# Kernel tuning notes

Hardware: AMD Instinct MI355X
Metric: run time of the kernel (lower is better)

Reference implementation:

```python
import jax, jax.numpy as jnp
import numpy as np

E = 1024      # embed_dim
H = 16        # num heads
D = E // H    # head_dim = 64
B, T = 4, 2048


def setup_inputs() -> dict:
    key = jax.random.key(0)
    ks = jax.random.split(key, 7)
    hidden_states = jax.random.normal(ks[0], (B, T, E), dtype=jnp.float32)
    # torch Linear weight layout: [out_features, in_features]
    Wqkv = jax.random.normal(ks[1], (3 * E, E), dtype=jnp.float32) * (1.0 / np.sqrt(E))
    bqkv = jax.random.normal(ks[2], (3 * E,), dtype=jnp.float32) * 0.02
    Wproj = jax.random.normal(ks[3], (E, E), dtype=jnp.float32) * (1.0 / np.sqrt(E))
    bproj = jax.random.normal(ks[4], (E,), dtype=jnp.float32) * 0.02
    splat_scale = jax.random.normal(ks[5], (H,), dtype=jnp.float32) * 0.5
    splat_bias = jax.random.normal(ks[6], (H, 1, 1), dtype=jnp.float32) * 0.5
    return {
        'hidden_states': hidden_states,
        'Wqkv': Wqkv, 'bqkv': bqkv,
        'Wproj': Wproj, 'bproj': bproj,
        'splat_scale': splat_scale, 'splat_bias': splat_bias,
    }


def reference(hidden_states, Wqkv, bqkv, Wproj, bproj, splat_scale, splat_bias):
    b, t, _ = hidden_states.shape
    scale_factor = 1.0 / np.sqrt(D)

    qkv = hidden_states @ Wqkv.T + bqkv                    # [B,T,3E]
    q, k, v = jnp.split(qkv, 3, axis=-1)
    # [B,H,T,D]
    q = q.reshape(b, t, H, D).transpose(0, 2, 1, 3)
    k = k.reshape(b, t, H, D).transpose(0, 2, 1, 3)
    v = v.reshape(b, t, H, D).transpose(0, 2, 1, 3)

    scores = jnp.einsum('bhqd,bhkd->bhqk', q * scale_factor, k)  # [B,H,T,T]

    s = (1.0 + 0.01 * jnp.tanh(splat_scale)).reshape(1, H, 1, 1)
    bsp = (0.001 * jnp.tanh(splat_bias)).reshape(1, H, 1, 1)
    scores = s * scores + bsp

    causal = jnp.tril(jnp.ones((t, t), dtype=bool))
    scores = jnp.where(causal, scores, jnp.float32(-1e9))

    attn = jax.nn.softmax(scores, axis=-1)                 # dropout = identity (eval)
    out = jnp.einsum('bhqk,bhkd->bhqd', attn, v)
    out = out.transpose(0, 2, 1, 3).reshape(b, t, E)
    out = out @ Wproj.T + bproj
    return out
```

## Files before the change

### kernel.cpp

```cpp
#include <hip/hip_runtime.h>
#include <stdint.h>

#define BB 4
#define TT 2048
#define EE 1024
#define HH 16
#define DD 64
#define MM (BB*TT)
#define NQKV (3*EE)

typedef __bf16 bf16_t;
typedef bf16_t bf16x8 __attribute__((ext_vector_type(8)));
typedef short  s16x4  __attribute__((ext_vector_type(4)));
typedef float  floatx4 __attribute__((ext_vector_type(4)));

__device__ __forceinline__ unsigned short f2bf(float f) {
    unsigned int u = __float_as_uint(f);
    u = (u + 0x7FFFu + ((u >> 16) & 1u)) >> 16;
    return (unsigned short)u;
}

__device__ __forceinline__ void load_lds16(const void* g, void* l) {
    __builtin_amdgcn_global_load_lds(
        (const __attribute__((address_space(1))) unsigned int*)g,
        (__attribute__((address_space(3))) unsigned int*)l, 16, 0, 0);
}

__global__ void cvt_f32_bf16(const float* __restrict__ in,
                             unsigned short* __restrict__ out, int n) {
    int i = (blockIdx.x * 256 + threadIdx.x) * 4;
    if (i + 3 < n) {
        float4 v = *reinterpret_cast<const float4*>(in + i);
        ushort4 o;
        o.x = f2bf(v.x); o.y = f2bf(v.y); o.z = f2bf(v.z); o.w = f2bf(v.w);
        *reinterpret_cast<ushort4*>(out + i) = o;
    }
}

template<int N, int K, int EPI>
__global__ __launch_bounds__(256, 3) void gemm_bt(
    const unsigned short* __restrict__ A,
    const unsigned short* __restrict__ Bw,
    const float* __restrict__ bias,
    const float* __restrict__ sscale,
    unsigned short* __restrict__ Qb,
    unsigned short* __restrict__ Kb,
    unsigned short* __restrict__ Vtb,
    float* __restrict__ Cout)
{
    __shared__ __align__(16) unsigned short As[128 * 32];
    __shared__ __align__(16) unsigned short Bs[128 * 32];
    __shared__ float qsc[16];

    const int tid  = threadIdx.x;
    const int lane = tid & 63;
    const int w    = tid >> 6;
    const int quad = lane >> 4;
    const int l16  = lane & 15;
    const int m0   = blockIdx.y * 128;
    const int n0   = blockIdx.x * 128;
    const int wm   = (w & 1) * 64;
    const int wn   = (w >> 1) * 64;

    if (EPI == 0 && tid < 16) qsc[tid] = (1.0f + 0.01f * tanhf(sscale[tid])) * 0.125f;

    floatx4 acc[4][4] = {};

    for (int kk = 0; kk < K; kk += 32) {
        __syncthreads();
#pragma unroll
        for (int c = 0; c < 2; ++c) {
            int idx = c * 256 + tid;
            const unsigned short* ga = A  + (size_t)(m0 + (idx >> 2)) * K + kk + (idx & 3) * 8;
            load_lds16(ga, &As[(c * 256 + w * 64) * 8]);
            const unsigned short* gb = Bw + (size_t)(n0 + (idx >> 2)) * K + kk + (idx & 3) * 8;
            load_lds16(gb, &Bs[(c * 256 + w * 64) * 8]);
        }
        __syncthreads();

        bf16x8 af[4], bfr[4];
#pragma unroll
        for (int mt = 0; mt < 4; ++mt)
            af[mt] = *reinterpret_cast<const bf16x8*>(&As[(wm + mt * 16 + l16) * 32 + quad * 8]);
#pragma unroll
        for (int nt = 0; nt < 4; ++nt)
            bfr[nt] = *reinterpret_cast<const bf16x8*>(&Bs[(wn + nt * 16 + l16) * 32 + quad * 8]);
#pragma unroll
        for (int mt = 0; mt < 4; ++mt)
#pragma unroll
            for (int nt = 0; nt < 4; ++nt)
                acc[mt][nt] = __builtin_amdgcn_mfma_f32_16x16x32_bf16(af[mt], bfr[nt], acc[mt][nt], 0, 0, 0);
    }

    if (EPI == 0) {
#pragma unroll
        for (int mt = 0; mt < 4; ++mt) {
            int rowb = m0 + wm + mt * 16 + quad * 4;
#pragma unroll
            for (int nt = 0; nt < 4; ++nt) {
                int col = n0 + wn + nt * 16 + l16;
                int which = col >> 10;
                int e = col & 1023;
                int h = e >> 6, d = e & 63;
                float bsv = bias[col];
#pragma unroll
                for (int r = 0; r < 4; ++r) {
                    int m = rowb + r;
                    int b = m >> 11, t = m & 2047;
                    float v = acc[mt][nt][r] + bsv;
                    size_t bh = (size_t)(b * HH + h);
                    if (which == 0) {
                        v *= qsc[h];
                        Qb[(bh * TT + t) * DD + d] = f2bf(v);
                    } else if (which == 1) {
                        Kb[(bh * TT + t) * DD + d] = f2bf(v);
                    } else {
                        Vtb[(bh * DD + d) * TT + t] = f2bf(v);
                    }
                }
            }
        }
    } else {
#pragma unroll
        for (int mt = 0; mt < 4; ++mt) {
            int rowb = m0 + wm + mt * 16 + quad * 4;
#pragma unroll
            for (int nt = 0; nt < 4; ++nt) {
                int col = n0 + wn + nt * 16 + l16;
                float bsv = bias[col];
#pragma unroll
                for (int r = 0; r < 4; ++r)
                    Cout[(size_t)(rowb + r) * N + col] = acc[mt][nt][r] + bsv;
            }
        }
    }
}

#define LP 72
__global__ __launch_bounds__(256, 3) void flash_attn(
    const unsigned short* __restrict__ Qb,
    const unsigned short* __restrict__ Kb,
    const unsigned short* __restrict__ Vtb,
    unsigned short* __restrict__ Ob)
{
    __shared__ __align__(16) unsigned short Ks[2][64 * LP];
    __shared__ __align__(16) unsigned short Vs[2][64 * LP];

    const int tid  = threadIdx.x;
    const int lane = tid & 63;
    const int w    = tid >> 6;
    const int quad = lane >> 4;
    const int l16  = lane & 15;
    const int bh   = blockIdx.y;
    const int qt   = 15 - blockIdx.x;
    const int row0 = qt * 128 + w * 32;

    const unsigned short* qbase = &Qb[((size_t)bh * TT + row0 + l16) * DD + quad * 8];
    const bf16x8 qf00 = *reinterpret_cast<const bf16x8*>(qbase);
    const bf16x8 qf01 = *reinterpret_cast<const bf16x8*>(qbase + 32);
    const bf16x8 qf10 = *reinterpret_cast<const bf16x8*>(qbase + 16 * DD);
    const bf16x8 qf11 = *reinterpret_cast<const bf16x8*>(qbase + 16 * DD + 32);

    const s16x4 vones = { (short)0x3F80, (short)0x3F80, (short)0x3F80, (short)0x3F80 };

    floatx4 o[2][4] = {};
    floatx4 o1[2] = {};

    const int ktmax = 2 * qt + 1;

    const int srow = tid >> 3;
    const int scol = (tid & 7) * 8;
    const size_t kgbase = ((size_t)bh * TT + srow) * DD + scol;
    const size_t vgbase = ((size_t)bh * DD + srow) * TT + scol;

    uint4 kr0 = *reinterpret_cast<const uint4*>(&Kb[kgbase]);
    uint4 kr1 = *reinterpret_cast<const uint4*>(&Kb[kgbase + 32 * DD]);
    uint4 vr0 = *reinterpret_cast<const uint4*>(&Vtb[vgbase]);
    uint4 vr1 = *reinterpret_cast<const uint4*>(&Vtb[vgbase + 32 * TT]);

    for (int kt = 0; kt <= ktmax; ++kt) {
        const int buf = kt & 1;
        *reinterpret_cast<uint4*>(&Ks[buf][srow * LP + scol]) = kr0;
        *reinterpret_cast<uint4*>(&Ks[buf][(srow + 32) * LP + scol]) = kr1;
        *reinterpret_cast<uint4*>(&Vs[buf][srow * LP + scol]) = vr0;
        *reinterpret_cast<uint4*>(&Vs[buf][(srow + 32) * LP + scol]) = vr1;
        __syncthreads();

        if (kt < ktmax) {
            size_t ko = kgbase + (size_t)(kt + 1) * 64 * DD;
            size_t vo = vgbase + (size_t)(kt + 1) * 64;
            kr0 = *reinterpret_cast<const uint4*>(&Kb[ko]);
            kr1 = *reinterpret_cast<const uint4*>(&Kb[ko + 32 * DD]);
            vr0 = *reinterpret_cast<const uint4*>(&Vtb[vo]);
            vr1 = *reinterpret_cast<const uint4*>(&Vtb[vo + 32 * TT]);
        }

        if (kt * 64 <= row0 + 31) {
            const int keyb = kt * 64 + quad * 4;
            const int qr0  = row0 + l16;

#pragma unroll
            for (int ntk = 0; ntk < 4; ++ntk) {
                const unsigned short* krow = &Ks[buf][(ntk * 16 + l16) * LP + quad * 8];
                bf16x8 kf0 = *reinterpret_cast<const bf16x8*>(krow);
                bf16x8 kf1 = *reinterpret_cast<const bf16x8*>(krow + 32);

                floatx4 st0 = {0.f, 0.f, 0.f, 0.f};
                floatx4 st1 = {0.f, 0.f, 0.f, 0.f};
                st0 = __builtin_amdgcn_mfma_f32_16x16x32_bf16(kf0, qf00, st0, 0, 0, 0);
                st0 = __builtin_amdgcn_mfma_f32_16x16x32_bf16(kf1, qf01, st0, 0, 0, 0);
                st1 = __builtin_amdgcn_mfma_f32_16x16x32_bf16(kf0, qf10, st1, 0, 0, 0);
                st1 = __builtin_amdgcn_mfma_f32_16x16x32_bf16(kf1, qf11, st1, 0, 0, 0);

                s16x4 pf0, pf1;
#pragma unroll
                for (int r = 0; r < 4; ++r) {
                    int key = keyb + ntk * 16 + r;
                    float p0 = __expf(st0[r]);
                    pf0[r] = (short)((key <= qr0) ? f2bf(p0) : 0);
                    float p1 = __expf(st1[r]);
                    pf1[r] = (short)((key <= qr0 + 16) ? f2bf(p1) : 0);
                }

                o1[0] = __builtin_amdgcn_mfma_f32_16x16x16bf16_1k(pf0, vones, o1[0], 0, 0, 0);
                o1[1] = __builtin_amdgcn_mfma_f32_16x16x16bf16_1k(pf1, vones, o1[1], 0, 0, 0);
#pragma unroll
                for (int dt = 0; dt < 4; ++dt) {
                    s16x4 vf = *reinterpret_cast<const s16x4*>(
                        &Vs[buf][(dt * 16 + l16) * LP + ntk * 16 + quad * 4]);
                    o[0][dt] = __builtin_amdgcn_mfma_f32_16x16x16bf16_1k(pf0, vf, o[0][dt], 0, 0, 0);
                    o[1][dt] = __builtin_amdgcn_mfma_f32_16x16x16bf16_1k(pf1, vf, o[1][dt], 0, 0, 0);
                }
            }
        }
    }

    const int b = bh >> 4, h = bh & 15;
#pragma unroll
    for (int mt = 0; mt < 2; ++mt) {
#pragma unroll
        for (int r = 0; r < 4; ++r) {
            int q = row0 + mt * 16 + quad * 4 + r;
            float rl = __builtin_amdgcn_rcpf(o1[mt][r]);
#pragma unroll
            for (int dt = 0; dt < 4; ++dt)
                Ob[((size_t)(b * TT + q)) * EE + h * DD + dt * 16 + l16] =
                    f2bf(o[mt][dt][r] * rl);
        }
    }
}

extern "C" void kernel_launch(void* const* d_in, const int* in_sizes, int n_in,
                              void* d_out, int out_size, void* d_ws, size_t ws_size,
                              hipStream_t stream) {
    const float* hs    = (const float*)d_in[0];
    const float* Wqkv  = (const float*)d_in[1];
    const float* bqkv  = (const float*)d_in[2];
    const float* Wproj = (const float*)d_in[3];
    const float* bproj = (const float*)d_in[4];
    const float* ss    = (const float*)d_in[5];
    float* out = (float*)d_out;

    char* p = (char*)d_ws;
    unsigned short* hsb    = (unsigned short*)p; p += (size_t)MM * EE * 2;
    unsigned short* wqkvb  = (unsigned short*)p; p += (size_t)NQKV * EE * 2;
    unsigned short* wprojb = (unsigned short*)p; p += (size_t)EE * EE * 2;
    unsigned short* Qb     = (unsigned short*)p; p += (size_t)BB*HH*TT*DD * 2;
    unsigned short* Kb     = (unsigned short*)p; p += (size_t)BB*HH*TT*DD * 2;
    unsigned short* Vtb    = (unsigned short*)p; p += (size_t)BB*HH*TT*DD * 2;

    cvt_f32_bf16<<<(MM * EE) / 1024, 256, 0, stream>>>(hs, hsb, MM * EE);
    cvt_f32_bf16<<<(NQKV * EE) / 1024, 256, 0, stream>>>(Wqkv, wqkvb, NQKV * EE);
    cvt_f32_bf16<<<(EE * EE) / 1024, 256, 0, stream>>>(Wproj, wprojb, EE * EE);

    gemm_bt<NQKV, EE, 0><<<dim3(NQKV / 128, MM / 128), 256, 0, stream>>>(
        hsb, wqkvb, bqkv, ss, Qb, Kb, Vtb, nullptr);

    flash_attn<<<dim3(TT / 128, BB * HH), 256, 0, stream>>>(Qb, Kb, Vtb, hsb);

    gemm_bt<EE, EE, 1><<<dim3(EE / 128, MM / 128), 256, 0, stream>>>(
        hsb, wprojb, bproj, nullptr, nullptr, nullptr, nullptr, out);
}
```

Measured before the change: 329.0 us.

## Shrink attention query tile to 64 rows with flattened heavy-first grid

```diff
diff --git a/kernel.cpp b/kernel.cpp
--- a/kernel.cpp
+++ b/kernel.cpp
@@ -137,7 +137,7 @@
 }
 
 #define LP 72
-__global__ __launch_bounds__(256, 3) void flash_attn(
+__global__ __launch_bounds__(256, 4) void flash_attn(
     const unsigned short* __restrict__ Qb,
     const unsigned short* __restrict__ Kb,
     const unsigned short* __restrict__ Vtb,
@@ -151,22 +151,19 @@
     const int w    = tid >> 6;
     const int quad = lane >> 4;
     const int l16  = lane & 15;
-    const int bh   = blockIdx.y;
-    const int qt   = 15 - blockIdx.x;
-    const int row0 = qt * 128 + w * 32;
+    const int i    = blockIdx.x;
+    const int bh   = i & 63;
+    const int qt   = 31 - (i >> 6);
+    const int row0 = qt * 64 + w * 16;
 
     const unsigned short* qbase = &Qb[((size_t)bh * TT + row0 + l16) * DD + quad * 8];
-    const bf16x8 qf00 = *reinterpret_cast<const bf16x8*>(qbase);
-    const bf16x8 qf01 = *reinterpret_cast<const bf16x8*>(qbase + 32);
-    const bf16x8 qf10 = *reinterpret_cast<const bf16x8*>(qbase + 16 * DD);
-    const bf16x8 qf11 = *reinterpret_cast<const bf16x8*>(qbase + 16 * DD + 32);
+    const bf16x8 qf0 = *reinterpret_cast<const bf16x8*>(qbase);
+    const bf16x8 qf1 = *reinterpret_cast<const bf16x8*>(qbase + 32);
 
     const s16x4 vones = { (short)0x3F80, (short)0x3F80, (short)0x3F80, (short)0x3F80 };
 
-    floatx4 o[2][4] = {};
-    floatx4 o1[2] = {};
-
-    const int ktmax = 2 * qt + 1;
+    floatx4 o[4] = {};
+    floatx4 o1 = {};
 
     const int srow = tid >> 3;
     const int scol = (tid & 7) * 8;
@@ -178,7 +175,7 @@
     uint4 vr0 = *reinterpret_cast<const uint4*>(&Vtb[vgbase]);
     uint4 vr1 = *reinterpret_cast<const uint4*>(&Vtb[vgbase + 32 * TT]);
 
-    for (int kt = 0; kt <= ktmax; ++kt) {
+    for (int kt = 0; kt <= qt; ++kt) {
         const int buf = kt & 1;
         *reinterpret_cast<uint4*>(&Ks[buf][srow * LP + scol]) = kr0;
         *reinterpret_cast<uint4*>(&Ks[buf][(srow + 32) * LP + scol]) = kr1;
@@ -186,7 +183,7 @@
         *reinterpret_cast<uint4*>(&Vs[buf][(srow + 32) * LP + scol]) = vr1;
         __syncthreads();
 
-        if (kt < ktmax) {
+        if (kt < qt) {
             size_t ko = kgbase + (size_t)(kt + 1) * 64 * DD;
             size_t vo = vgbase + (size_t)(kt + 1) * 64;
             kr0 = *reinterpret_cast<const uint4*>(&Kb[ko]);
@@ -195,58 +192,46 @@
             vr1 = *reinterpret_cast<const uint4*>(&Vtb[vo + 32 * TT]);
         }
 
-        if (kt * 64 <= row0 + 31) {
-            const int keyb = kt * 64 + quad * 4;
-            const int qr0  = row0 + l16;
-
-#pragma unroll
-            for (int ntk = 0; ntk < 4; ++ntk) {
-                const unsigned short* krow = &Ks[buf][(ntk * 16 + l16) * LP + quad * 8];
-                bf16x8 kf0 = *reinterpret_cast<const bf16x8*>(krow);
-                bf16x8 kf1 = *reinterpret_cast<const bf16x8*>(krow + 32);
-
-                floatx4 st0 = {0.f, 0.f, 0.f, 0.f};
-                floatx4 st1 = {0.f, 0.f, 0.f, 0.f};
-                st0 = __builtin_amdgcn_mfma_f32_16x16x32_bf16(kf0, qf00, st0, 0, 0, 0);
-                st0 = __builtin_amdgcn_mfma_f32_16x16x32_bf16(kf1, qf01, st0, 0, 0, 0);
-                st1 = __builtin_amdgcn_mfma_f32_16x16x32_bf16(kf0, qf10, st1, 0, 0, 0);
-                st1 = __builtin_amdgcn_mfma_f32_16x16x32_bf16(kf1, qf11, st1, 0, 0, 0);
-
-                s16x4 pf0, pf1;
-#pragma unroll
-                for (int r = 0; r < 4; ++r) {
-                    int key = keyb + ntk * 16 + r;
-                    float p0 = __expf(st0[r]);
-                    pf0[r] = (short)((key <= qr0) ? f2bf(p0) : 0);
-                    float p1 = __expf(st1[r]);
-                    pf1[r] = (short)((key <= qr0 + 16) ? f2bf(p1) : 0);
-                }
-
-                o1[0] = __builtin_amdgcn_mfma_f32_16x16x16bf16_1k(pf0, vones, o1[0], 0, 0, 0);
-                o1[1] = __builtin_amdgcn_mfma_f32_16x16x16bf16_1k(pf1, vones, o1[1], 0, 0, 0);
-#pragma unroll
-                for (int dt = 0; dt < 4; ++dt) {
-                    s16x4 vf = *reinterpret_cast<const s16x4*>(
-                        &Vs[buf][(dt * 16 + l16) * LP + ntk * 16 + quad * 4]);
-                    o[0][dt] = __builtin_amdgcn_mfma_f32_16x16x16bf16_1k(pf0, vf, o[0][dt], 0, 0, 0);
-                    o[1][dt] = __builtin_amdgcn_mfma_f32_16x16x16bf16_1k(pf1, vf, o[1][dt], 0, 0, 0);
-                }
+        const int keyb = kt * 64 + quad * 4;
+        const int qr0  = row0 + l16;
+        const bool diag = (kt == qt);
+
+#pragma unroll
+        for (int ntk = 0; ntk < 4; ++ntk) {
+            const unsigned short* krow = &Ks[buf][(ntk * 16 + l16) * LP + quad * 8];
+            bf16x8 kf0 = *reinterpret_cast<const bf16x8*>(krow);
+            bf16x8 kf1 = *reinterpret_cast<const bf16x8*>(krow + 32);
+
+            floatx4 st = {0.f, 0.f, 0.f, 0.f};
+            st = __builtin_amdgcn_mfma_f32_16x16x32_bf16(kf0, qf0, st, 0, 0, 0);
+            st = __builtin_amdgcn_mfma_f32_16x16x32_bf16(kf1, qf1, st, 0, 0, 0);
+
+            s16x4 pf;
+#pragma unroll
+            for (int r = 0; r < 4; ++r) {
+                float p = __expf(st[r]);
+                pf[r] = (short)((!diag || (keyb + ntk * 16 + r <= qr0)) ? f2bf(p) : 0);
+            }
+
+            o1 = __builtin_amdgcn_mfma_f32_16x16x16bf16_1k(pf, vones, o1, 0, 0, 0);
+#pragma unroll
+            for (int dt = 0; dt < 4; ++dt) {
+                s16x4 vf = *reinterpret_cast<const s16x4*>(
+                    &Vs[buf][(dt * 16 + l16) * LP + ntk * 16 + quad * 4]);
+                o[dt] = __builtin_amdgcn_mfma_f32_16x16x16bf16_1k(pf, vf, o[dt], 0, 0, 0);
             }
         }
     }
 
     const int b = bh >> 4, h = bh & 15;
 #pragma unroll
-    for (int mt = 0; mt < 2; ++mt) {
-#pragma unroll
-        for (int r = 0; r < 4; ++r) {
-            int q = row0 + mt * 16 + quad * 4 + r;
-            float rl = __builtin_amdgcn_rcpf(o1[mt][r]);
-#pragma unroll
-            for (int dt = 0; dt < 4; ++dt)
-                Ob[((size_t)(b * TT + q)) * EE + h * DD + dt * 16 + l16] =
-                    f2bf(o[mt][dt][r] * rl);
-        }
+    for (int r = 0; r < 4; ++r) {
+        int q = row0 + quad * 4 + r;
+        float rl = __builtin_amdgcn_rcpf(o1[r]);
+#pragma unroll
+        for (int dt = 0; dt < 4; ++dt)
+            Ob[((size_t)(b * TT + q)) * EE + h * DD + dt * 16 + l16] =
+                f2bf(o[dt][r] * rl);
     }
 }
 
@@ -276,7 +261,7 @@
     gemm_bt<NQKV, EE, 0><<<dim3(NQKV / 128, MM / 128), 256, 0, stream>>>(
         hsb, wqkvb, bqkv, ss, Qb, Kb, Vtb, nullptr);
 
-    flash_attn<<<dim3(TT / 128, BB * HH), 256, 0, stream>>>(Qb, Kb, Vtb, hsb);
+    flash_attn<<<dim3(2048), 256, 0, stream>>>(Qb, Kb, Vtb, hsb);
 
     gemm_bt<EE, EE, 1><<<dim3(EE / 128, MM / 128), 256, 0, stream>>>(
         hsb, wprojb, bproj, nullptr, nullptr, nullptr, nullptr, out);
```

Measured after the change: 287.0 us. 1.15x faster.
